# Kernel tuning notes

Hardware: AMD Instinct MI355X
Metric: run time of the kernel (lower is better)

## Reference

```python
import jax, jax.numpy as jnp
import numpy as np
import math

DIM = 1024
N_HEAD = 16
HEAD_DIM = DIM // N_HEAD  # 64
B, T = 4, 2048


def rotate_half(x):
    # lucidrains-style interleaved rotation: (x1, x2) pairs -> (-x2, x1)
    x = x.reshape(*x.shape[:-1], -1, 2)
    x1, x2 = x[..., 0], x[..., 1]
    return jnp.stack((-x2, x1), axis=-1).reshape(*x.shape[:-2], -1)


def apply_rope(x):
    # x: [b, h, t, d]
    d = x.shape[-1]
    t = x.shape[-2]
    inv_freq = 1.0 / (10000.0 ** (jnp.arange(0, d, 2, dtype=jnp.float32) / d))  # [d/2]
    angles = jnp.arange(t, dtype=jnp.float32)[:, None] * inv_freq[None, :]      # [t, d/2]
    angles = jnp.repeat(angles, 2, axis=-1)                                     # [t, d] interleaved
    cos, sin = jnp.cos(angles), jnp.sin(angles)
    return x * cos + rotate_half(x) * sin


def setup_inputs() -> dict:
    key = jax.random.key(0)
    kx, kw1, kb1, kw2, kb2 = jax.random.split(key, 5)
    x = jax.random.normal(kx, (B, T, DIM), dtype=jnp.float32)
    mask = jnp.tril(jnp.ones((T, T), dtype=jnp.int32))  # causal
    s = 0.02
    qkv_w = jax.random.normal(kw1, (DIM, 3 * DIM), dtype=jnp.float32) * s
    qkv_b = jax.random.normal(kb1, (3 * DIM,), dtype=jnp.float32) * s
    out_w = jax.random.normal(kw2, (DIM, DIM), dtype=jnp.float32) * s
    out_b = jax.random.normal(kb2, (DIM,), dtype=jnp.float32) * s
    return {"x": x, "mask": mask, "qkv_w": qkv_w, "qkv_b": qkv_b,
            "out_w": out_w, "out_b": out_b}


def reference(x, mask, qkv_w, qkv_b, out_w, out_b):
    b, t, _ = x.shape
    qkv = x @ qkv_w + qkv_b                       # [b, t, 3*dim]
    q, k, v = jnp.split(qkv, 3, axis=-1)
    def to_heads(z):
        return z.reshape(b, t, N_HEAD, HEAD_DIM).transpose(0, 2, 1, 3)  # [b,h,t,d]
    q, k, v = to_heads(q), to_heads(k), to_heads(v)
    q = apply_rope(q)
    k = apply_rope(k)
    scores = jnp.einsum('bhqd,bhkd->bhqk', q, k) / math.sqrt(HEAD_DIM)
    scores = jnp.where(mask[None, None, :, :] == 0, -jnp.inf, scores)
    attn = jax.nn.softmax(scores, axis=-1)        # dropout = identity (eval)
    out = jnp.einsum('bhqk,bhkd->bhqd', attn, v)  # [b,h,t,d]
    out = out.transpose(0, 2, 1, 3).reshape(b, t, DIM)
    return out @ out_w + out_b
```

## Files before the change

kernel.cpp:

```cpp
#include <hip/hip_runtime.h>

typedef __bf16 bf16_t;
typedef __bf16 bf16x8 __attribute__((ext_vector_type(8)));
typedef float  f32x4  __attribute__((ext_vector_type(4)));
typedef float  f32x16 __attribute__((ext_vector_type(16)));
typedef unsigned u32x4 __attribute__((ext_vector_type(4)));

#define DIMM  1024
#define NHEAD 16
#define HDIM  64
#define BATCH 4
#define SEQ   2048
#define MROWS (BATCH*SEQ)

#define AQB   128
#define AKV   64
#define NP    (SEQ/AQB)
#define SKS   72
#define LOG2E 1.44269504088896f

__device__ __forceinline__ void gload_lds16(const bf16_t* g, bf16_t* l) {
  __builtin_amdgcn_global_load_lds(
      (const __attribute__((address_space(1))) void*)g,
      (__attribute__((address_space(3))) void*)l, 16, 0, 0);
}

__device__ __forceinline__ unsigned short f2bu(float f) {
  bf16_t b = (bf16_t)f;
  return __builtin_bit_cast(unsigned short, b);
}
__device__ __forceinline__ float bu2f(unsigned short u) {
  return __uint_as_float(((unsigned)u) << 16);
}
__device__ __forceinline__ unsigned packbf(float a, float b) {
  return (unsigned)f2bu(a) | ((unsigned)f2bu(b) << 16);
}
__device__ __forceinline__ float fexp2(float x) {
  float r; asm("v_exp_f32 %0, %1" : "=v"(r) : "v"(x)); return r;
}

__global__ void k_convert(const float* __restrict__ in, bf16_t* __restrict__ out, int n4) {
  int i = blockIdx.x * blockDim.x + threadIdx.x;
  if (i >= n4) return;
  float4 v = reinterpret_cast<const float4*>(in)[i];
  ushort4 o;
  o.x = f2bu(v.x); o.y = f2bu(v.y); o.z = f2bu(v.z); o.w = f2bu(v.w);
  reinterpret_cast<ushort4*>(out)[i] = o;
}

__global__ void k_transpose_convert(const float* __restrict__ in, bf16_t* __restrict__ out,
                                    int R, int C) {
  __shared__ float tile[32][33];
  int cb = blockIdx.x * 32, rb = blockIdx.y * 32;
  int tx = threadIdx.x, ty = threadIdx.y;
  #pragma unroll
  for (int i = 0; i < 4; ++i)
    tile[ty + i*8][tx] = in[(size_t)(rb + ty + i*8) * C + cb + tx];
  __syncthreads();
  #pragma unroll
  for (int i = 0; i < 4; ++i)
    out[(size_t)(cb + ty + i*8) * R + rb + tx] = (bf16_t)tile[tx][ty + i*8];
}

__global__ void k_rope_table(float* __restrict__ cosT, float* __restrict__ sinT) {
  int id = blockIdx.x * blockDim.x + threadIdx.x;
  if (id >= SEQ * 32) return;
  int t = id >> 5, i = id & 31;
  double ang = (double)t * pow(10000.0, -(double)i / 32.0);
  cosT[id] = (float)cos(ang);
  sinT[id] = (float)sin(ang);
}

__global__ __launch_bounds__(512, 2) void k_gemm0(
    const bf16_t* __restrict__ A, const bf16_t* __restrict__ BT,
    const float* __restrict__ bias,
    bf16_t* __restrict__ q, bf16_t* __restrict__ k, bf16_t* __restrict__ vt,
    const float* __restrict__ cosT, const float* __restrict__ sinT)
{
  __shared__ bf16_t sA[2][2][128 * 64];
  __shared__ bf16_t sB[2][2][128 * 64];

  const int tid = threadIdx.x;
  const int w = tid >> 6;
  const int lane = tid & 63;
  const int wm = w >> 2, wn = w & 3;
  const int l15 = lane & 15, l4 = lane >> 4;

  int nwg = gridDim.x * gridDim.y;
  int id  = blockIdx.y * gridDim.x + blockIdx.x;
  int cpx = nwg >> 3;
  int sid = (id & 7) * cpx + (id >> 3);
  int bx = sid % gridDim.x, by = sid / gridDim.x;
  const int rowA0 = by * 256, colB0 = bx * 256;

  f32x4 acc[8][4] = {};
  bf16x8 bf_[4];

  auto stage = [&](int tile, int part) {
    if (tile >= 16) return;
    const int kh = part >> 1;
    const bool isB = part & 1;
    const bf16_t* src = isB ? BT : A;
    const int r0 = isB ? colB0 : rowA0;
    bf16_t* dst = (isB ? &sB[0][0][0] : &sA[0][0][0]) + ((tile & 1) * 2 + kh) * (128 * 64);
    #pragma unroll
    for (int call = 0; call < 2; ++call) {
      int n = call * 512 + tid;
      int R = n >> 3, slot = n & 7;
      int sp = slot ^ (R & 7);
      int row = R * 2 + (sp >> 2);
      gload_lds16(src + (size_t)(r0 + row) * 1024 + tile * 64 + kh * 32 + (sp & 3) * 8,
                  dst + n * 8);
    }
  };

  auto rdA = [&](int bc, int kh, int mfa) -> bf16x8 {
    int row = wm * 128 + mfa * 16 + l15;
    int R = row >> 1;
    int slot = (((row & 1) << 2) | l4) ^ (R & 7);
    return *reinterpret_cast<const bf16x8*>(&sA[bc][kh][R * 64 + slot * 8]);
  };
  auto rdB = [&](int bc, int kh, int nf) -> bf16x8 {
    int row = wn * 64 + nf * 16 + l15;
    int R = row >> 1;
    int slot = (((row & 1) << 2) | l4) ^ (R & 7);
    return *reinterpret_cast<const bf16x8*>(&sB[bc][kh][R * 64 + slot * 8]);
  };

  auto phase = [&](int bc, int kh, int mh, int stile, int spart, int wait_n) {
    bf16x8 af[4];
    if (mh == 0) {
      #pragma unroll
      for (int nf = 0; nf < 4; ++nf) bf_[nf] = rdB(bc, kh, nf);
    }
    #pragma unroll
    for (int mf = 0; mf < 4; ++mf) af[mf] = rdA(bc, kh, mh * 4 + mf);
    stage(stile, spart);
    if (wait_n == 4)      asm volatile("s_waitcnt vmcnt(4)" ::: "memory");
    else if (wait_n == 0) asm volatile("s_waitcnt vmcnt(0)" ::: "memory");
    __builtin_amdgcn_s_barrier();
    __builtin_amdgcn_s_setprio(1);
    #pragma unroll
    for (int mf = 0; mf < 4; ++mf)
      #pragma unroll
      for (int nf = 0; nf < 4; ++nf)
        acc[mh * 4 + mf][nf] = __builtin_amdgcn_mfma_f32_16x16x32_bf16(
            af[mf], bf_[nf], acc[mh * 4 + mf][nf], 0, 0, 0);
    __builtin_amdgcn_s_setprio(0);
    __builtin_amdgcn_s_barrier();
  };

  stage(0, 0); stage(0, 1); stage(0, 2); stage(0, 3);
  stage(1, 0); stage(1, 1);
  asm volatile("s_waitcnt vmcnt(4)" ::: "memory");
  __builtin_amdgcn_s_barrier();

  for (int i = 0; i < 8; ++i) {
    const int t0 = 2 * i, t1 = 2 * i + 1;
    phase(0, 0, 0, t1,     2, -1);
    phase(0, 0, 1, t1,     3, -1);
    phase(0, 1, 0, t0 + 2, 0, -1);
    phase(0, 1, 1, t0 + 2, 1, (t0 + 2 < 16) ? 4 : 0);
    phase(1, 0, 0, t0 + 2, 2, -1);
    phase(1, 0, 1, t0 + 2, 3, -1);
    phase(1, 1, 0, t0 + 3, 0, -1);
    phase(1, 1, 1, t0 + 3, 1, (t0 + 3 < 16) ? 4 : 0);
  }

  const bool isV = (bx >= 8);
  const bool isQ = (bx < 4);
  const float qs = 0.125f * LOG2E;
  if (isV) {
    #pragma unroll
    for (int mfa = 0; mfa < 8; ++mfa) {
      #pragma unroll
      for (int nf = 0; nf < 4; ++nf) {
        int n = colB0 + wn * 64 + nf * 16 + l15;
        int h = (n >> 6) & 15, d = n & 63;
        float bs = bias[n];
        int m0 = rowA0 + wm * 128 + mfa * 16 + l4 * 4;
        int b = m0 >> 11, t = m0 & 2047;
        ushort4 pk;
        pk.x = f2bu(acc[mfa][nf][0] + bs);
        pk.y = f2bu(acc[mfa][nf][1] + bs);
        pk.z = f2bu(acc[mfa][nf][2] + bs);
        pk.w = f2bu(acc[mfa][nf][3] + bs);
        *reinterpret_cast<ushort4*>(
            vt + ((size_t)((b * NHEAD + h) * HDIM + d)) * SEQ + t) = pk;
      }
    }
  } else {
    bf16_t* dst = isQ ? q : k;
    #pragma unroll
    for (int mfa = 0; mfa < 8; ++mfa) {
      #pragma unroll
      for (int nf = 0; nf < 4; ++nf) {
        int n = colB0 + wn * 64 + nf * 16 + l15;
        int h = (n >> 6) & 15, d = n & 63;
        int i2 = d >> 1;
        float bs = bias[n];
        #pragma unroll
        for (int r = 0; r < 4; ++r) {
          int m = rowA0 + wm * 128 + mfa * 16 + l4 * 4 + r;
          int b = m >> 11, t = m & 2047;
          float val = acc[mfa][nf][r] + bs;
          float prt = __shfl_xor(val, 1);
          float c = cosT[(t << 5) + i2], s = sinT[(t << 5) + i2];
          float y = (d & 1) ? (val * c + prt * s) : (val * c - prt * s);
          if (isQ) y *= qs;
          dst[((size_t)(b * NHEAD + h) * SEQ + t) * HDIM + d] = (bf16_t)y;
        }
      }
    }
  }
}

__global__ __launch_bounds__(256) void k_gemm1(
    const bf16_t* __restrict__ A, const bf16_t* __restrict__ BT,
    const float* __restrict__ bias, float* __restrict__ outf, int M, int N, int K)
{
  __shared__ bf16_t sA[128 * 32];
  __shared__ bf16_t sB[128 * 32];
  const int tid = threadIdx.x;
  const int w = tid >> 6, lane = tid & 63;
  const int wr = w >> 1, wc = w & 1;
  const int l15 = lane & 15, l4 = lane >> 4;

  int nwg = gridDim.x * gridDim.y;
  int id  = blockIdx.y * gridDim.x + blockIdx.x;
  int cpx = nwg >> 3;
  int sid = (id & 7) * cpx + (id >> 3);
  int bx = sid % gridDim.x, by = sid / gridDim.x;

  const int rowA0 = by * 128;
  const int colB0 = bx * 128;

  f32x4 acc[4][4] = {};

  const int nkt = K >> 5;
  for (int kt = 0; kt < nkt; ++kt) {
    __syncthreads();
    #pragma unroll
    for (int i = 0; i < 2; ++i) {
      int c = i * 256 + w * 64 + lane;
      int row = c >> 2, k8 = (c & 3) * 8;
      gload_lds16(A  + (size_t)(rowA0 + row) * K + kt * 32 + k8, sA + (i * 256 + w * 64) * 8);
      gload_lds16(BT + (size_t)(colB0 + row) * K + kt * 32 + k8, sB + (i * 256 + w * 64) * 8);
    }
    asm volatile("s_waitcnt vmcnt(0)" ::: "memory");
    __syncthreads();
    bf16x8 af[4], bfr[4];
    #pragma unroll
    for (int mi = 0; mi < 4; ++mi)
      af[mi] = *reinterpret_cast<const bf16x8*>(sA + (wr * 64 + mi * 16 + l15) * 32 + l4 * 8);
    #pragma unroll
    for (int ni = 0; ni < 4; ++ni)
      bfr[ni] = *reinterpret_cast<const bf16x8*>(sB + (wc * 64 + ni * 16 + l15) * 32 + l4 * 8);
    #pragma unroll
    for (int mi = 0; mi < 4; ++mi)
      #pragma unroll
      for (int ni = 0; ni < 4; ++ni)
        acc[mi][ni] = __builtin_amdgcn_mfma_f32_16x16x32_bf16(af[mi], bfr[ni], acc[mi][ni], 0, 0, 0);
  }

  #pragma unroll
  for (int mi = 0; mi < 4; ++mi) {
    #pragma unroll
    for (int ni = 0; ni < 4; ++ni) {
      int n = colB0 + wc * 64 + ni * 16 + l15;
      float bs = bias[n];
      #pragma unroll
      for (int r = 0; r < 4; ++r) {
        int m = rowA0 + wr * 64 + mi * 16 + l4 * 4 + r;
        outf[(size_t)m * N + n] = acc[mi][ni][r] + bs;
      }
    }
  }
}

#define ATTN_BODY(CBUF, T)                                                     \
  do {                                                                         \
    const int t_ = (T);                                                        \
    if (t_ + 1 < nt) {                                                         \
      asm volatile("s_waitcnt vmcnt(0)" ::: "memory");                         \
      stage(CBUF ^ 1);                                                         \
      if (t_ + 2 < nt) issue(t_ + 2);                                          \
    }                                                                          \
    const bool masked = (t_ * AKV + AKV - 1 > qbase);                          \
    _Pragma("unroll")                                                          \
    for (int sub = 0; sub < 2; ++sub) {                                        \
      f32x16 sc = {};                                                          \
      __builtin_amdgcn_s_setprio(1);                                           \
      _Pragma("unroll")                                                        \
      for (int kt = 0; kt < 4; ++kt) {                                         \
        int krow = 32 * sub + l31;                                             \
        bf16x8 kf = *reinterpret_cast<const bf16x8*>(                          \
            &sK[CBUF][krow * SKS + (((2 * kt + hi) ^ (krow >> 3)) << 3)]);     \
        sc = __builtin_amdgcn_mfma_f32_32x32x16_bf16(kf, qf[kt], sc, 0, 0, 0); \
      }                                                                        \
      __builtin_amdgcn_s_setprio(0);                                           \
      float p[16];                                                             \
      const int qa = qbase + l31;                                              \
      const int kb0 = t_ * AKV + 32 * sub + 4 * hi;                            \
      _Pragma("unroll")                                                        \
      for (int r = 0; r < 16; ++r) {                                           \
        float s = sc[r];                                                       \
        if (masked) {                                                          \
          int kvi = kb0 + (r & 3) + 8 * (r >> 2);                              \
          if (kvi > qa) s = -1e30f;                                            \
        }                                                                      \
        p[r] = s;                                                              \
      }                                                                        \
      float m0 = fmaxf(fmaxf(p[0],  p[1]),  p[2]);                             \
      float m1 = fmaxf(fmaxf(p[3],  p[4]),  p[5]);                             \
      float m2 = fmaxf(fmaxf(p[6],  p[7]),  p[8]);                             \
      float m3 = fmaxf(fmaxf(p[9],  p[10]), p[11]);                            \
      float m4 = fmaxf(fmaxf(p[12], p[13]), p[14]);                            \
      float mt = fmaxf(fmaxf(fmaxf(m0, m1), fmaxf(m2, m3)), fmaxf(m4, p[15]));\
      mt = fmaxf(mt, __shfl_xor(mt, 32));                                      \
      if (!__all(mt <= mrun + 11.54f)) {                                       \
        float mnew = fmaxf(mrun, mt);                                          \
        float scl = fexp2(mrun - mnew);                                        \
        mrun = mnew;                                                           \
        lrun *= scl;                                                           \
        _Pragma("unroll")                                                      \
        for (int i = 0; i < 16; ++i) { accO[0][i] *= scl; accO[1][i] *= scl; } \
      }                                                                        \
      float rs = 0.f;                                                          \
      _Pragma("unroll")                                                        \
      for (int r = 0; r < 16; ++r) { p[r] = fexp2(p[r] - mrun); rs += p[r]; }  \
      lrun += rs + __shfl_xor(rs, 32);                                         \
      bf16x8 pf[2];                                                            \
      _Pragma("unroll")                                                        \
      for (int kt = 0; kt < 2; ++kt) {                                         \
        unsigned P01 = packbf(p[8*kt+0], p[8*kt+1]);                           \
        unsigned P23 = packbf(p[8*kt+2], p[8*kt+3]);                           \
        unsigned P45 = packbf(p[8*kt+4], p[8*kt+5]);                           \
        unsigned P67 = packbf(p[8*kt+6], p[8*kt+7]);                           \
        unsigned ra = __shfl_xor(hi == 0 ? P45 : P01, 32);                     \
        unsigned rb = __shfl_xor(hi == 0 ? P67 : P23, 32);                     \
        unsigned dw0 = hi == 0 ? P01 : ra;                                     \
        unsigned dw1 = hi == 0 ? P23 : rb;                                     \
        unsigned dw2 = hi == 0 ? ra : P45;                                     \
        unsigned dw3 = hi == 0 ? rb : P67;                                     \
        pf[kt] = __builtin_bit_cast(bf16x8, (u32x4){dw0, dw1, dw2, dw3});      \
      }                                                                        \
      __builtin_amdgcn_s_setprio(1);                                           \
      _Pragma("unroll")                                                        \
      for (int dt = 0; dt < 2; ++dt) {                                         \
        _Pragma("unroll")                                                      \
        for (int kt = 0; kt < 2; ++kt) {                                       \
          int vrow = 32 * dt + l31;                                            \
          bf16x8 vf = *reinterpret_cast<const bf16x8*>(                        \
              &sV[CBUF][vrow * SKS + (((4 * sub + 2 * kt + hi) ^ (vrow >> 3)) << 3)]); \
          accO[dt] = __builtin_amdgcn_mfma_f32_32x32x16_bf16(vf, pf[kt], accO[dt], 0, 0, 0); \
        }                                                                      \
      }                                                                        \
      __builtin_amdgcn_s_setprio(0);                                           \
    }                                                                          \
    asm volatile("s_waitcnt lgkmcnt(0)" ::: "memory");                         \
    __builtin_amdgcn_s_barrier();                                              \
    asm volatile("" ::: "memory");                                             \
  } while (0)

__global__ __launch_bounds__(256, 2) void k_attn(
    const bf16_t* __restrict__ Q, const bf16_t* __restrict__ Kb,
    const bf16_t* __restrict__ Vt, bf16_t* __restrict__ O)
{
  __shared__ bf16_t sK[2][64 * SKS];
  __shared__ bf16_t sV[2][64 * SKS];

  const int tid = threadIdx.x;
  const int w = tid >> 6, lane = tid & 63;
  const int l31 = lane & 31, hi = lane >> 5;

  const int id = blockIdx.x;
  const int j4 = id >> 8;
  const int k4 = (id >> 6) & 3;
  const int bh = id & 63;
  const int qblk = (j4 == 0) ? 15 - 2 * k4
                 : (j4 == 1) ? 2 * k4
                 : (j4 == 2) ? 14 - 2 * k4
                 :             2 * k4 + 1;

  const size_t hbase = (size_t)bh * SEQ * HDIM;
  const int b = bh >> 4, h = bh & 15;
  const int srow = tid >> 3, sslot = tid & 7;

  const int qbase = qblk * AQB + 32 * w;
  const int nt = 2 * qblk + 2;

  bf16x8 qf[4];
  #pragma unroll
  for (int kt = 0; kt < 4; ++kt)
    qf[kt] = *reinterpret_cast<const bf16x8*>(
        Q + hbase + (size_t)(qbase + l31) * HDIM + kt * 16 + hi * 8);
  asm volatile("s_waitcnt vmcnt(0)" ::: "memory");
  asm volatile("" : "+v"(qf[0]), "+v"(qf[1]), "+v"(qf[2]), "+v"(qf[3]));

  u32x4 kr[2], vr[2];
  auto issue = [&](int t) {
    const bf16_t* kp = Kb + hbase + (size_t)(t * AKV + srow) * HDIM + sslot * 8;
    const bf16_t* vp = Vt + hbase + (size_t)srow * SEQ + t * AKV + sslot * 8;
    asm volatile("global_load_dwordx4 %0, %1, off" : "=v"(kr[0]) : "v"(kp));
    asm volatile("global_load_dwordx4 %0, %1, off" : "=v"(kr[1]) : "v"(kp + 32 * HDIM));
    asm volatile("global_load_dwordx4 %0, %1, off" : "=v"(vr[0]) : "v"(vp));
    asm volatile("global_load_dwordx4 %0, %1, off" : "=v"(vr[1]) : "v"(vp + 32 * SEQ));
  };
  auto stage = [&](int nb) {
    #pragma unroll
    for (int cc = 0; cc < 2; ++cc) {
      int row = srow + 32 * cc;
      *reinterpret_cast<u32x4*>(&sK[nb][row * SKS + ((sslot ^ (row >> 3)) << 3)]) = kr[cc];
      *reinterpret_cast<u32x4*>(&sV[nb][row * SKS + ((sslot ^ (row >> 3)) << 3)]) = vr[cc];
    }
  };

  float mrun = -1e30f, lrun = 0.f;
  f32x16 accO[2] = {};

  issue(0);
  asm volatile("s_waitcnt vmcnt(0)" ::: "memory");
  stage(0);
  issue(1);
  asm volatile("s_waitcnt lgkmcnt(0)" ::: "memory");
  __builtin_amdgcn_s_barrier();
  asm volatile("" ::: "memory");

  for (int tt = 0; tt < nt; tt += 2) {
    ATTN_BODY(0, tt);
    ATTN_BODY(1, tt + 1);
  }

  bf16_t* sOw = &sK[0][0] + w * (32 * SKS);
  float inv = 1.f / lrun;
  #pragma unroll
  for (int dt = 0; dt < 2; ++dt)
    #pragma unroll
    for (int r = 0; r < 16; ++r) {
      int d = 32 * dt + (r & 3) + 8 * (r >> 2) + 4 * hi;
      sOw[l31 * SKS + (d ^ ((l31 >> 3) << 3))] = (bf16_t)(accO[dt][r] * inv);
    }
  #pragma unroll
  for (int i = 0; i < 4; ++i) {
    int qr = 8 * i + (lane >> 3);
    int ch = lane & 7;
    bf16x8 vvv = *reinterpret_cast<const bf16x8*>(
        &sOw[qr * SKS + ((ch ^ (qr >> 3)) << 3)]);
    *reinterpret_cast<bf16x8*>(
        O + ((size_t)(b * SEQ + qbase + qr)) * DIMM + h * HDIM + ch * 8) = vvv;
  }
}

extern "C" void kernel_launch(void* const* d_in, const int* in_sizes, int n_in,
                              void* d_out, int out_size, void* d_ws, size_t ws_size,
                              hipStream_t stream) {
  const float* x     = (const float*)d_in[0];
  const float* qkv_w = (const float*)d_in[2];
  const float* qkv_b = (const float*)d_in[3];
  const float* out_w = (const float*)d_in[4];
  const float* out_b = (const float*)d_in[5];
  float* out = (float*)d_out;

  char* ws = (char*)d_ws;
  size_t off = 0;
  auto alloc = [&](size_t bytes) {
    char* p = ws + off;
    off += (bytes + 255) & ~(size_t)255;
    return (void*)p;
  };
  bf16_t* Xb    = (bf16_t*)alloc((size_t)MROWS * DIMM * 2);
  bf16_t* WqkvT = (bf16_t*)alloc((size_t)3 * DIMM * DIMM * 2);
  bf16_t* WoutT = (bf16_t*)alloc((size_t)DIMM * DIMM * 2);
  bf16_t* Qh    = (bf16_t*)alloc((size_t)64 * SEQ * HDIM * 2);
  bf16_t* Kh    = (bf16_t*)alloc((size_t)64 * SEQ * HDIM * 2);
  bf16_t* Vth   = (bf16_t*)alloc((size_t)64 * HDIM * SEQ * 2);
  bf16_t* AO    = (bf16_t*)alloc((size_t)MROWS * DIMM * 2);
  float*  cosT  = (float*)alloc((size_t)SEQ * 32 * 4);
  float*  sinT  = (float*)alloc((size_t)SEQ * 32 * 4);

  k_convert<<<(MROWS * DIMM / 4 + 255) / 256, 256, 0, stream>>>(x, Xb, MROWS * DIMM / 4);
  k_transpose_convert<<<dim3(3 * DIMM / 32, DIMM / 32), dim3(32, 8), 0, stream>>>(qkv_w, WqkvT, DIMM, 3 * DIMM);
  k_transpose_convert<<<dim3(DIMM / 32, DIMM / 32), dim3(32, 8), 0, stream>>>(out_w, WoutT, DIMM, DIMM);
  k_rope_table<<<(SEQ * 32 + 255) / 256, 256, 0, stream>>>(cosT, sinT);

  k_gemm0<<<dim3(3 * DIMM / 256, MROWS / 256), 512, 0, stream>>>(
      Xb, WqkvT, qkv_b, Qh, Kh, Vth, cosT, sinT);

  k_attn<<<dim3(NP * 64), 256, 0, stream>>>(Qh, Kh, Vth, AO);

  k_gemm1<<<dim3(DIMM / 128, MROWS / 128), 256, 0, stream>>>(
      AO, WoutT, out_b, out, MROWS, DIMM, DIMM);
}
```

Before: 194.1 us.

## Split long causal attention query blocks across two workgroups and merge partials

The attention kernel now splits the KV range of the eight longest query blocks (qblk 8-15) in half, so 24 work classes per head replace 16 and the work per block is more even. Split halves write bf16 partial outputs plus running max and sum to a workspace that reuses the X buffer. A new merge kernel combines the two halves with softmax rescaling. The goal is to shorten the tail of the causal load imbalance, at the cost of an extra launch, extra global traffic, and a bf16 rounding of the partials.

```diff
diff --git a/kernel.cpp b/kernel.cpp
--- a/kernel.cpp
+++ b/kernel.cpp
@@ -18,6 +18,9 @@
 #define NP    (SEQ/AQB)
 #define SKS   72
 #define LOG2E 1.44269504088896f
+
+__device__ const int d_qb[24] = {15,15,7,14,14,13,13,6,12,12,11,11,5,10,10,9,9,4,8,8,3,2,1,0};
+__device__ const int d_hh[24] = { 0, 1,2, 0, 1, 0, 1,2, 0, 1, 0, 1,2, 0, 1,0,1,2,0,1,2,2,2,2};
 
 __device__ __forceinline__ void gload_lds16(const bf16_t* g, bf16_t* l) {
   __builtin_amdgcn_global_load_lds(
@@ -281,10 +284,10 @@
 #define ATTN_BODY(CBUF, T)                                                     \
   do {                                                                         \
     const int t_ = (T);                                                        \
-    if (t_ + 1 < nt) {                                                         \
+    if (t_ + 1 < t1) {                                                         \
       asm volatile("s_waitcnt vmcnt(0)" ::: "memory");                         \
       stage(CBUF ^ 1);                                                         \
-      if (t_ + 2 < nt) issue(t_ + 2);                                          \
+      if (t_ + 2 < t1) issue(t_ + 2);                                          \
     }                                                                          \
     const bool masked = (t_ * AKV + AKV - 1 > qbase);                          \
     _Pragma("unroll")                                                          \
@@ -365,7 +368,8 @@
 
 __global__ __launch_bounds__(256, 2) void k_attn(
     const bf16_t* __restrict__ Q, const bf16_t* __restrict__ Kb,
-    const bf16_t* __restrict__ Vt, bf16_t* __restrict__ O)
+    const bf16_t* __restrict__ Vt, bf16_t* __restrict__ O,
+    bf16_t* __restrict__ Opart, float* __restrict__ ml)
 {
   __shared__ bf16_t sK[2][64 * SKS];
   __shared__ bf16_t sV[2][64 * SKS];
@@ -375,20 +379,19 @@
   const int l31 = lane & 31, hi = lane >> 5;
 
   const int id = blockIdx.x;
-  const int j4 = id >> 8;
-  const int k4 = (id >> 6) & 3;
+  const int cls = id >> 6;
   const int bh = id & 63;
-  const int qblk = (j4 == 0) ? 15 - 2 * k4
-                 : (j4 == 1) ? 2 * k4
-                 : (j4 == 2) ? 14 - 2 * k4
-                 :             2 * k4 + 1;
+  const int qblk = d_qb[cls];
+  const int hh = d_hh[cls];
+  const int ntf = 2 * qblk + 2;
+  const int t0 = (hh == 1) ? (ntf >> 1) : 0;
+  const int t1 = (hh == 0) ? (ntf >> 1) : ntf;
 
   const size_t hbase = (size_t)bh * SEQ * HDIM;
   const int b = bh >> 4, h = bh & 15;
   const int srow = tid >> 3, sslot = tid & 7;
 
   const int qbase = qblk * AQB + 32 * w;
-  const int nt = 2 * qblk + 2;
 
   bf16x8 qf[4];
   #pragma unroll
@@ -419,17 +422,20 @@
   float mrun = -1e30f, lrun = 0.f;
   f32x16 accO[2] = {};
 
-  issue(0);
+  issue(t0);
   asm volatile("s_waitcnt vmcnt(0)" ::: "memory");
   stage(0);
-  issue(1);
+  if (t0 + 1 < t1) issue(t0 + 1);
   asm volatile("s_waitcnt lgkmcnt(0)" ::: "memory");
   __builtin_amdgcn_s_barrier();
   asm volatile("" ::: "memory");
 
-  for (int tt = 0; tt < nt; tt += 2) {
-    ATTN_BODY(0, tt);
-    ATTN_BODY(1, tt + 1);
+  int t = t0;
+  if ((t1 - t0) & 1) {
+    ATTN_BODY(0, t); ++t;
+    for (; t < t1; t += 2) { ATTN_BODY(1, t); ATTN_BODY(0, t + 1); }
+  } else {
+    for (; t < t1; t += 2) { ATTN_BODY(0, t); ATTN_BODY(1, t + 1); }
   }
 
   bf16_t* sOw = &sK[0][0] + w * (32 * SKS);
@@ -441,14 +447,68 @@
       int d = 32 * dt + (r & 3) + 8 * (r >> 2) + 4 * hi;
       sOw[l31 * SKS + (d ^ ((l31 >> 3) << 3))] = (bf16_t)(accO[dt][r] * inv);
     }
+  if (hh == 2) {
+    #pragma unroll
+    for (int i = 0; i < 4; ++i) {
+      int qr = 8 * i + (lane >> 3);
+      int ch = lane & 7;
+      bf16x8 vvv = *reinterpret_cast<const bf16x8*>(
+          &sOw[qr * SKS + ((ch ^ (qr >> 3)) << 3)]);
+      *reinterpret_cast<bf16x8*>(
+          O + ((size_t)(b * SEQ + qbase + qr)) * DIMM + h * HDIM + ch * 8) = vvv;
+    }
+  } else {
+    const int pb = ((qblk - 8) * 2 + hh) * 64 + bh;
+    #pragma unroll
+    for (int i = 0; i < 4; ++i) {
+      int qr = 8 * i + (lane >> 3);
+      int ch = lane & 7;
+      bf16x8 vvv = *reinterpret_cast<const bf16x8*>(
+          &sOw[qr * SKS + ((ch ^ (qr >> 3)) << 3)]);
+      *reinterpret_cast<bf16x8*>(
+          Opart + ((size_t)pb * 128 + 32 * w + qr) * 64 + ch * 8) = vvv;
+    }
+    if (hi == 0) {
+      size_t mi = ((size_t)pb * 128 + 32 * w + l31) * 2;
+      ml[mi] = mrun; ml[mi + 1] = lrun;
+    }
+  }
+}
+
+__global__ __launch_bounds__(256) void k_merge(
+    const bf16_t* __restrict__ Opart, const float* __restrict__ ml,
+    bf16_t* __restrict__ O)
+{
+  int blk = blockIdx.x;
+  int qi = blk >> 6;
+  int bh = blk & 63;
+  int b = bh >> 4, h = bh & 15;
+  int qblk = qi + 8;
+  int base0 = (qi * 2 + 0) * 64 + bh;
+  int base1 = (qi * 2 + 1) * 64 + bh;
+  int q = threadIdx.x >> 1;
+  int d0 = (threadIdx.x & 1) * 32;
+
+  float m0 = ml[((size_t)base0 * 128 + q) * 2], l0 = ml[((size_t)base0 * 128 + q) * 2 + 1];
+  float m1 = ml[((size_t)base1 * 128 + q) * 2], l1 = ml[((size_t)base1 * 128 + q) * 2 + 1];
+  float m = fmaxf(m0, m1);
+  float w0 = fexp2(m0 - m) * l0;
+  float w1 = fexp2(m1 - m) * l1;
+  float inv = 1.f / (w0 + w1);
+  w0 *= inv; w1 *= inv;
+
+  const bf16_t* p0 = Opart + ((size_t)base0 * 128 + q) * 64 + d0;
+  const bf16_t* p1 = Opart + ((size_t)base1 * 128 + q) * 64 + d0;
+  bf16_t* po = O + ((size_t)(b * SEQ + qblk * 128 + q)) * DIMM + h * HDIM + d0;
   #pragma unroll
   for (int i = 0; i < 4; ++i) {
-    int qr = 8 * i + (lane >> 3);
-    int ch = lane & 7;
-    bf16x8 vvv = *reinterpret_cast<const bf16x8*>(
-        &sOw[qr * SKS + ((ch ^ (qr >> 3)) << 3)]);
-    *reinterpret_cast<bf16x8*>(
-        O + ((size_t)(b * SEQ + qbase + qr)) * DIMM + h * HDIM + ch * 8) = vvv;
+    bf16x8 a = *reinterpret_cast<const bf16x8*>(p0 + i * 8);
+    bf16x8 c = *reinterpret_cast<const bf16x8*>(p1 + i * 8);
+    bf16x8 o;
+    #pragma unroll
+    for (int j = 0; j < 8; ++j)
+      o[j] = (bf16_t)(w0 * (float)a[j] + w1 * (float)c[j]);
+    *reinterpret_cast<bf16x8*>(po + i * 8) = o;
   }
 }
 
@@ -478,6 +538,8 @@
   bf16_t* AO    = (bf16_t*)alloc((size_t)MROWS * DIMM * 2);
   float*  cosT  = (float*)alloc((size_t)SEQ * 32 * 4);
   float*  sinT  = (float*)alloc((size_t)SEQ * 32 * 4);
+  float*  mlbuf = (float*)alloc((size_t)16 * 64 * 128 * 2 * 4);
+  bf16_t* Opart = Xb;
 
   k_convert<<<(MROWS * DIMM / 4 + 255) / 256, 256, 0, stream>>>(x, Xb, MROWS * DIMM / 4);
   k_transpose_convert<<<dim3(3 * DIMM / 32, DIMM / 32), dim3(32, 8), 0, stream>>>(qkv_w, WqkvT, DIMM, 3 * DIMM);
@@ -487,7 +549,9 @@
   k_gemm0<<<dim3(3 * DIMM / 256, MROWS / 256), 512, 0, stream>>>(
       Xb, WqkvT, qkv_b, Qh, Kh, Vth, cosT, sinT);
 
-  k_attn<<<dim3(NP * 64), 256, 0, stream>>>(Qh, Kh, Vth, AO);
+  k_attn<<<dim3(24 * 64), 256, 0, stream>>>(Qh, Kh, Vth, AO, Opart, mlbuf);
+
+  k_merge<<<dim3(512), 256, 0, stream>>>(Opart, mlbuf, AO);
 
   k_gemm1<<<dim3(DIMM / 128, MROWS / 128), 256, 0, stream>>>(
       AO, WoutT, out_b, out, MROWS, DIMM, DIMM);
```

Result: no change. 195.5 us (+0.7%).
